# Kernel tuning notes

Hardware: AMD Instinct MI355X
Metric: run time of the kernel (lower is better)

## Reference

```python
import jax, jax.numpy as jnp
import numpy as np

B, S, E, H, F = 8, 1024, 1024, 16, 4096
D = E // H  # head_dim = 64
EPS = 1e-5


def setup_inputs() -> dict:
    key = jax.random.key(0)
    ks = jax.random.split(key, 12)
    s = 0.02
    return {
        "x": jax.random.normal(ks[0], (B, S, E), dtype=jnp.float32),
        # per-head projections (shared across heads), torch stores [out,in]; we use [in,out]
        "Wq": jax.random.normal(ks[1], (D, D), dtype=jnp.float32) * s,
        "Wk": jax.random.normal(ks[2], (D, D), dtype=jnp.float32) * s,
        "Wv": jax.random.normal(ks[3], (D, D), dtype=jnp.float32) * s,
        "Wo": jax.random.normal(ks[4], (E, E), dtype=jnp.float32) * s,
        "bo": jnp.zeros((E,), dtype=jnp.float32),
        "W1": jax.random.normal(ks[5], (E, F), dtype=jnp.float32) * s,
        "b1": jnp.zeros((F,), dtype=jnp.float32),
        "W2": jax.random.normal(ks[6], (F, E), dtype=jnp.float32) * s,
        "b2": jnp.zeros((E,), dtype=jnp.float32),
        "g1": jnp.ones((E,), dtype=jnp.float32),
        "beta1": jnp.zeros((E,), dtype=jnp.float32),
        "g2": jnp.ones((E,), dtype=jnp.float32),
        "beta2": jnp.zeros((E,), dtype=jnp.float32),
    }


def _layer_norm(x, g, b):
    m = jnp.mean(x, axis=-1, keepdims=True)
    v = jnp.mean(jnp.square(x - m), axis=-1, keepdims=True)
    return (x - m) * jax.lax.rsqrt(v + EPS) * g + b


def reference(x, Wq, Wk, Wv, Wo, bo, W1, b1, W2, b2, g1, beta1, g2, beta2):
    b, s, e = x.shape
    # --- attention sublayer (pre-norm) ---
    nx = _layer_norm(x, g1, beta1)
    h = nx.reshape(b, s, H, D)              # [B,S,H,D]
    q = h @ Wq                               # per-head linear, weight shared over heads
    k = h @ Wk
    v = h @ Wv
    energy = jnp.einsum('bqhd,bkhd->bhqk', q, k)  # full [B,H,S,S] scores
    mask = jnp.tril(jnp.ones((s, s), dtype=bool))
    energy = jnp.where(mask, energy, -jnp.inf)
    att = jax.nn.softmax(energy / jnp.sqrt(jnp.float32(e)), axis=-1)  # NOTE: scale by sqrt(embed_dim)
    o = jnp.einsum('bhqk,bkhd->bqhd', att, v).reshape(b, s, e)
    x = x + (o @ Wo + bo)
    # --- MLP sublayer (pre-norm); dropout is identity in eval ---
    nx = _layer_norm(x, g2, beta2)
    x = x + (jax.nn.relu(nx @ W1 + b1) @ W2 + b2)
    return x
```

## Files before the change

kernel.cpp:

```cpp
#include <hip/hip_runtime.h>

typedef unsigned short u16;
typedef __attribute__((ext_vector_type(4))) float f4;
typedef __attribute__((ext_vector_type(8))) short s8v;
typedef __attribute__((ext_vector_type(4))) unsigned short u16x4;

#define DEVINL __device__ __forceinline__

DEVINL float b2f(u16 u) { union { unsigned i; float f; } x; x.i = ((unsigned)u) << 16; return x.f; }
DEVINL u16 f2b(float f) {
  union { float f; unsigned i; } x; x.f = f;
  unsigned r = 0x7FFFu + ((x.i >> 16) & 1u);
  return (u16)((x.i + r) >> 16);
}

#define GLD_LDS16(g, l)                                                        \
  __builtin_amdgcn_global_load_lds((__attribute__((address_space(1))) void*)(g), \
                                   (__attribute__((address_space(3))) void*)(l), 16, 0, 0)

__global__ __launch_bounds__(256) void k_transpose_all(
    const float* __restrict__ Wo, const float* __restrict__ W1,
    const float* __restrict__ W2, const float* __restrict__ Wq,
    const float* __restrict__ Wk, const float* __restrict__ Wv,
    u16* __restrict__ WoT, u16* __restrict__ W1T, u16* __restrict__ W2T,
    u16* __restrict__ WqT, u16* __restrict__ WkT, u16* __restrict__ WvT) {
  int id = blockIdx.x;
  const float* in;
  u16* out;
  int R, C, bx, by;
  if (id < 1024) {
    in = Wo; out = WoT; R = 1024; C = 1024; bx = id & 31; by = id >> 5;
  } else if (id < 5120) {
    int t = id - 1024;
    in = W1; out = W1T; R = 1024; C = 4096; bx = t & 127; by = t >> 7;
  } else if (id < 9216) {
    int t = id - 5120;
    in = W2; out = W2T; R = 4096; C = 1024; bx = t & 31; by = t >> 5;
  } else {
    int t = id - 9216;
    int z = t >> 2;
    in = z == 0 ? Wq : (z == 1 ? Wk : Wv);
    out = z == 0 ? WqT : (z == 1 ? WkT : WvT);
    R = 64; C = 64; bx = t & 1; by = (t >> 1) & 1;
  }
  __shared__ float tt[32][33];
  int tx = threadIdx.x & 31, ty = threadIdx.x >> 5;
  int c0 = bx * 32, r0 = by * 32;
#pragma unroll
  for (int i = 0; i < 32; i += 8)
    tt[ty + i][tx] = in[(long)(r0 + ty + i) * C + (c0 + tx)];
  __syncthreads();
#pragma unroll
  for (int i = 0; i < 32; i += 8)
    out[(long)(c0 + ty + i) * R + (r0 + tx)] = f2b(tt[tx][ty + i]);
}

__global__ __launch_bounds__(256) void k_vtrans(const u16* __restrict__ v, u16* __restrict__ vt) {
  __shared__ u16 t[64][72];
  int bh = blockIdx.x, b = bh >> 4, h = bh & 15;
  int s0 = blockIdx.y * 64;
  int tid = threadIdx.x;
#pragma unroll
  for (int p = 0; p < 2; ++p) {
    int idx = p * 256 + tid;
    int sl = idx >> 3, c8 = (idx & 7) * 8;
    *(s8v*)(&t[sl][c8]) = *(const s8v*)(v + (((long)(b * 1024 + s0 + sl) * 16 + h) * 64) + c8);
  }
  __syncthreads();
#pragma unroll
  for (int p = 0; p < 2; ++p) {
    int idx = p * 256 + tid;
    int d = idx >> 3, c8 = (idx & 7) * 8;
    s8v o;
#pragma unroll
    for (int e = 0; e < 8; ++e) o[e] = (short)t[c8 + e][d];
    *(s8v*)(vt + ((long)bh * 64 + d) * 1024 + s0 + c8) = o;
  }
}

__global__ __launch_bounds__(256) void k_layernorm(const float* __restrict__ x,
                                                   const float* __restrict__ g,
                                                   const float* __restrict__ be,
                                                   u16* __restrict__ out) {
  long row = blockIdx.x;
  int tid = threadIdx.x;
  f4 v = ((const f4*)(x + row * 1024))[tid];
  float s = v[0] + v[1] + v[2] + v[3];
  float s2 = v[0] * v[0] + v[1] * v[1] + v[2] * v[2] + v[3] * v[3];
#pragma unroll
  for (int off = 32; off > 0; off >>= 1) {
    s += __shfl_down(s, off, 64);
    s2 += __shfl_down(s2, off, 64);
  }
  __shared__ float red[8];
  int wv = tid >> 6, ln = tid & 63;
  if (ln == 0) { red[wv] = s; red[4 + wv] = s2; }
  __syncthreads();
  s = red[0] + red[1] + red[2] + red[3];
  s2 = red[4] + red[5] + red[6] + red[7];
  float mean = s * (1.0f / 1024.0f);
  float var = s2 * (1.0f / 1024.0f) - mean * mean;
  float rs = rsqrtf(var + 1e-5f);
  f4 gg = ((const f4*)g)[tid];
  f4 bb = ((const f4*)be)[tid];
  u16x4 o;
#pragma unroll
  for (int i = 0; i < 4; ++i) o[i] = f2b((v[i] - mean) * rs * gg[i] + bb[i]);
  ((u16x4*)(out + row * 1024))[tid] = o;
}

__global__ __launch_bounds__(256) void k_ln_qkv(
    const float* __restrict__ x, const float* __restrict__ g, const float* __restrict__ be,
    const u16* __restrict__ WqT, const u16* __restrict__ WkT, const u16* __restrict__ WvT,
    u16* __restrict__ q, u16* __restrict__ k, u16* __restrict__ v) {
  constexpr int LDP = 72;
  __shared__ u16 A[64 * LDP];
  int tid = threadIdx.x, lane = tid & 63, wave = tid >> 6;
  int quad = lane >> 4, l16 = lane & 15;
  long xrow = (long)blockIdx.x * 4 + wave;
  const f4* xp = (const f4*)(x + xrow * 1024);
  const f4* gp = (const f4*)g;
  const f4* bp = (const f4*)be;
  f4 vv[4];
  float s = 0.f, s2 = 0.f;
#pragma unroll
  for (int j = 0; j < 4; ++j) {
    vv[j] = xp[lane * 4 + j];
#pragma unroll
    for (int e = 0; e < 4; ++e) { s += vv[j][e]; s2 += vv[j][e] * vv[j][e]; }
  }
#pragma unroll
  for (int off = 1; off < 64; off <<= 1) {
    s += __shfl_xor(s, off, 64);
    s2 += __shfl_xor(s2, off, 64);
  }
  float mean = s * (1.0f / 1024.0f);
  float var = s2 * (1.0f / 1024.0f) - mean * mean;
  float rs = rsqrtf(var + 1e-5f);
  u16* ap = &A[(wave * 16 + (lane >> 2)) * LDP + (lane & 3) * 16];
#pragma unroll
  for (int j = 0; j < 4; ++j) {
    f4 gg = gp[lane * 4 + j], bb = bp[lane * 4 + j];
    u16x4 o;
#pragma unroll
    for (int e = 0; e < 4; ++e) o[e] = f2b((vv[j][e] - mean) * rs * gg[e] + bb[e]);
    *(u16x4*)(ap + j * 4) = o;
  }
  __syncthreads();
  s8v a0 = *(const s8v*)(&A[(wave * 16 + l16) * LDP + quad * 8]);
  s8v a1 = *(const s8v*)(&A[(wave * 16 + l16) * LDP + 32 + quad * 8]);
  long rbase = (long)blockIdx.x * 64 + wave * 16;
  const u16* Ws[3] = {WqT, WkT, WvT};
  u16* Os[3] = {q, k, v};
#pragma unroll
  for (int t = 0; t < 3; ++t) {
    f4 acc4[4];
#pragma unroll
    for (int j = 0; j < 4; ++j) {
      s8v b0 = *(const s8v*)(Ws[t] + (j * 16 + l16) * 64 + quad * 8);
      s8v b1 = *(const s8v*)(Ws[t] + (j * 16 + l16) * 64 + 32 + quad * 8);
      f4 acc = {0.f, 0.f, 0.f, 0.f};
      acc = __builtin_amdgcn_mfma_f32_16x16x32_bf16(a0, b0, acc, 0, 0, 0);
      acc = __builtin_amdgcn_mfma_f32_16x16x32_bf16(a1, b1, acc, 0, 0, 0);
      acc4[j] = acc;
    }
    __syncthreads();
#pragma unroll
    for (int j = 0; j < 4; ++j)
#pragma unroll
      for (int r = 0; r < 4; ++r)
        A[(wave * 16 + quad * 4 + r) * LDP + j * 16 + l16] = f2b(acc4[j][r]);
    __syncthreads();
#pragma unroll
    for (int it = 0; it < 2; ++it) {
      int idx = it * 64 + lane;
      int row = idx >> 3, c8 = (idx & 7) * 8;
      s8v v8 = *(const s8v*)(&A[(wave * 16 + row) * LDP + c8]);
      *(s8v*)(Os[t] + (rbase + row) * 64 + c8) = v8;
    }
  }
}

__global__ __launch_bounds__(512) void k_attn_mfma(const u16* __restrict__ q,
                                                   const u16* __restrict__ kk,
                                                   const u16* __restrict__ vt,
                                                   u16* __restrict__ o) {
  constexpr int LDK = 72;
  __shared__ u16 Ks[2][64 * LDK];
  __shared__ u16 Vt[2][64 * LDK];
  __shared__ u16 Ps[8][16 * LDK];
  int tid = threadIdx.x, lane = tid & 63, wave = tid >> 6;
  int quad = lane >> 4, l16 = lane & 15;
  int b = blockIdx.x >> 4, h = blockIdx.x & 15;
  int qi = (int)gridDim.y - 1 - (int)blockIdx.y;
  int q0 = qi * 128 + wave * 16;
  int myNt = 2 * qi + (wave >> 2);
  int lastKt = 2 * qi + 1;

  const u16* qp = q + (((long)(b * 1024 + q0 + l16)) * 16 + h) * 64;
  s8v aq0 = *(const s8v*)(qp + quad * 8);
  s8v aq1 = *(const s8v*)(qp + 32 + quad * 8);

  int srow = tid >> 3, sc8 = (tid & 7) * 8;
  const u16* kb_ = kk + (long)b * 1048576 + h * 64;
  const u16* vb_ = vt + (long)blockIdx.x * 65536;

  f4 O[4];
  float m_[4], l_[4];
#pragma unroll
  for (int jd = 0; jd < 4; ++jd) O[jd] = f4{0.f, 0.f, 0.f, 0.f};
#pragma unroll
  for (int r = 0; r < 4; ++r) { m_[r] = -__builtin_inff(); l_[r] = 0.f; }

  s8v rk0 = *(const s8v*)(kb_ + (long)srow * 1024 + sc8);
  s8v rv0 = *(const s8v*)(vb_ + (long)srow * 1024 + sc8);
  *(s8v*)(&Ks[0][srow * LDK + sc8]) = rk0;
  *(s8v*)(&Vt[0][srow * LDK + sc8]) = rv0;

  for (int kt = 0; kt <= lastKt; ++kt) {
    int cur = kt & 1;
    if (kt < lastKt) {
      long ko = (long)(kt + 1) * 64;
      rk0 = *(const s8v*)(kb_ + (ko + srow) * 1024 + sc8);
      rv0 = *(const s8v*)(vb_ + (long)srow * 1024 + (kt + 1) * 64 + sc8);
    }
    __syncthreads();

    if (kt <= myNt) {
      const u16* Kc = Ks[cur];
      const u16* Vc = Vt[cur];
      f4 sf[4];
      __builtin_amdgcn_s_setprio(1);
#pragma unroll
      for (int jn = 0; jn < 4; ++jn) {
        s8v b0 = *(const s8v*)(Kc + (jn * 16 + l16) * LDK + quad * 8);
        s8v b1 = *(const s8v*)(Kc + (jn * 16 + l16) * LDK + 32 + quad * 8);
        f4 acc = f4{0.f, 0.f, 0.f, 0.f};
        acc = __builtin_amdgcn_mfma_f32_16x16x32_bf16(aq0, b0, acc, 0, 0, 0);
        acc = __builtin_amdgcn_mfma_f32_16x16x32_bf16(aq1, b1, acc, 0, 0, 0);
        sf[jn] = acc;
      }
      __builtin_amdgcn_s_setprio(0);
      bool diag = (kt == myNt);
      int rloc = (wave & 3) * 16 + quad * 4;
      float rm[4];
#pragma unroll
      for (int r = 0; r < 4; ++r) rm[r] = -__builtin_inff();
#pragma unroll
      for (int jn = 0; jn < 4; ++jn)
#pragma unroll
        for (int r = 0; r < 4; ++r) {
          float v = sf[jn][r] * 0.03125f;
          if (diag && (jn * 16 + l16 > rloc + r)) v = -__builtin_inff();
          sf[jn][r] = v;
          rm[r] = fmaxf(rm[r], v);
        }
#pragma unroll
      for (int off = 1; off < 16; off <<= 1)
#pragma unroll
        for (int r = 0; r < 4; ++r) rm[r] = fmaxf(rm[r], __shfl_xor(rm[r], off, 64));
      bool ok = (rm[0] <= m_[0] + 8.f) && (rm[1] <= m_[1] + 8.f) &&
                (rm[2] <= m_[2] + 8.f) && (rm[3] <= m_[3] + 8.f);
      if (!__all(ok)) {
#pragma unroll
        for (int r = 0; r < 4; ++r) {
          float mn = fmaxf(m_[r], rm[r]);
          float alpha = __expf(m_[r] - mn);
          m_[r] = mn;
          l_[r] *= alpha;
#pragma unroll
          for (int jd = 0; jd < 4; ++jd) O[jd][r] *= alpha;
        }
      }
      float rs[4];
#pragma unroll
      for (int r = 0; r < 4; ++r) rs[r] = 0.f;
#pragma unroll
      for (int jn = 0; jn < 4; ++jn)
#pragma unroll
        for (int r = 0; r < 4; ++r) {
          float p = __expf(sf[jn][r] - m_[r]);
          rs[r] += p;
          Ps[wave][(quad * 4 + r) * LDK + jn * 16 + l16] = f2b(p);
        }
#pragma unroll
      for (int off = 1; off < 16; off <<= 1)
#pragma unroll
        for (int r = 0; r < 4; ++r) rs[r] += __shfl_xor(rs[r], off, 64);
#pragma unroll
      for (int r = 0; r < 4; ++r) l_[r] += rs[r];
      asm volatile("s_waitcnt lgkmcnt(0)" ::: "memory");
      s8v p0 = *(const s8v*)(&Ps[wave][l16 * LDK + quad * 8]);
      s8v p1 = *(const s8v*)(&Ps[wave][l16 * LDK + 32 + quad * 8]);
      __builtin_amdgcn_s_setprio(1);
#pragma unroll
      for (int jd = 0; jd < 4; ++jd) {
        s8v b0 = *(const s8v*)(Vc + (jd * 16 + l16) * LDK + quad * 8);
        s8v b1 = *(const s8v*)(Vc + (jd * 16 + l16) * LDK + 32 + quad * 8);
        O[jd] = __builtin_amdgcn_mfma_f32_16x16x32_bf16(p0, b0, O[jd], 0, 0, 0);
        O[jd] = __builtin_amdgcn_mfma_f32_16x16x32_bf16(p1, b1, O[jd], 0, 0, 0);
      }
      __builtin_amdgcn_s_setprio(0);
    }

    if (kt < lastKt) {
      int nb = (cur ^ 1);
      *(s8v*)(&Ks[nb][srow * LDK + sc8]) = rk0;
      *(s8v*)(&Vt[nb][srow * LDK + sc8]) = rv0;
    }
  }
  __syncthreads();
#pragma unroll
  for (int r = 0; r < 4; ++r) {
    float inv = 1.0f / l_[r];
#pragma unroll
    for (int jd = 0; jd < 4; ++jd)
      Ps[wave][(quad * 4 + r) * LDK + jd * 16 + l16] = f2b(O[jd][r] * inv);
  }
  __syncthreads();
#pragma unroll
  for (int it = 0; it < 2; ++it) {
    int idx = it * 64 + lane;
    int row = idx >> 3, c8 = (idx & 7) * 8;
    s8v v8 = *(const s8v*)(&Ps[wave][row * LDK + c8]);
    *(s8v*)(o + (((long)(b * 1024 + q0 + row)) * 16 + h) * 64 + c8) = v8;
  }
}

template <int EPI>
__global__ __launch_bounds__(512) void k_gemm256(const u16* __restrict__ A,
                                                 const u16* __restrict__ BT,
                                                 const float* __restrict__ bias,
                                                 const float* __restrict__ resid,
                                                 void* __restrict__ outp, int M, int N, int K,
                                                 int lda) {
  __shared__ __align__(16) u16 S[65536];
  int tid = threadIdx.x, lane = tid & 63, wave = tid >> 6;
  int l16 = lane & 15, quad = lane >> 4;
  int wm = wave >> 2, wn = wave & 3;
  long bm = blockIdx.x, bn = blockIdx.y;
  int z = blockIdx.z;

  int rl = l16 & 7;
  int c0 = 8 * (quad ^ rl);
  int c1 = 8 * ((quad ^ 4) ^ rl);
  int rowA = (wm * 64 + l16) * 64;
  int rowB = (wn * 32 + l16) * 64;

  int Lb = tid * 16;
  int Ls = Lb ^ (((Lb >> 7) & 7) << 4);
  int r_ = Ls >> 7, kin = (Ls & 127) >> 1;
  const u16* pA = A + (bm * 256 + r_) * (long)lda + kin + (long)z * K;
  const u16* pB = BT + (bn * 256 + r_) * (long)lda + kin + (long)z * K;

  f4 acc[4][4][2];
#pragma unroll
  for (int q = 0; q < 4; ++q)
#pragma unroll
    for (int mi = 0; mi < 4; ++mi)
#pragma unroll
      for (int nj = 0; nj < 2; ++nj) acc[q][mi][nj] = f4{0.f, 0.f, 0.f, 0.f};
  s8v aF[4][2], bF[2][2][2];

#define BAR asm volatile("s_barrier" ::: "memory")
#define LGK0 asm volatile("s_waitcnt lgkmcnt(0)" ::: "memory")
#define WVM4 asm volatile("s_waitcnt vmcnt(4)" ::: "memory")
#define WVM0 asm volatile("s_waitcnt vmcnt(0)" ::: "memory")

#define STAGE(mat, half, t, buf)                                               \
  do {                                                                         \
    const u16* g_ = ((mat) ? pB : pA) + (long)(half) * 128 * lda + (t) * 64;   \
    char* l_ = ((char*)S) + ((buf) * 32768 + (mat) * 16384 + (half) * 8192) * 2 + wave * 1024; \
    GLD_LDS16(g_, l_);                                                         \
    GLD_LDS16(g_ + 64 * (long)lda, l_ + 8192);                                 \
  } while (0)

#define LDA(buf, mh)                                                           \
  do {                                                                         \
    const u16* p_ = S + (buf) * 32768 + (mh) * 8192 + rowA;                    \
    _Pragma("unroll") for (int mi = 0; mi < 4; ++mi) {                         \
      aF[mi][0] = *(const s8v*)(p_ + mi * 1024 + c0);                          \
      aF[mi][1] = *(const s8v*)(p_ + mi * 1024 + c1);                          \
    }                                                                          \
  } while (0)

#define LDB(buf, nh, set)                                                      \
  do {                                                                         \
    const u16* p_ = S + (buf) * 32768 + 16384 + (nh) * 8192 + rowB;            \
    _Pragma("unroll") for (int nj = 0; nj < 2; ++nj) {                         \
      bF[set][nj][0] = *(const s8v*)(p_ + nj * 1024 + c0);                     \
      bF[set][nj][1] = *(const s8v*)(p_ + nj * 1024 + c1);                     \
    }                                                                          \
  } while (0)

#define MM(q)                                                                  \
  do {                                                                         \
    _Pragma("unroll") for (int mi = 0; mi < 4; ++mi)                           \
        _Pragma("unroll") for (int nj = 0; nj < 2; ++nj) {                     \
      acc[q][mi][nj] = __builtin_amdgcn_mfma_f32_16x16x32_bf16(                \
          aF[mi][0], bF[(q) & 1][nj][0], acc[q][mi][nj], 0, 0, 0);             \
      acc[q][mi][nj] = __builtin_amdgcn_mfma_f32_16x16x32_bf16(                \
          aF[mi][1], bF[(q) & 1][nj][1], acc[q][mi][nj], 0, 0, 0);             \
    }                                                                          \
  } while (0)

#define PHASES(t, LAST)                                                        \
  LDA(0, 0); LDB(0, 0, 0); STAGE(0, 1, (t) + 1, 1);                            \
  BAR; LGK0; __builtin_amdgcn_s_setprio(1); MM(0); __builtin_amdgcn_s_setprio(0); BAR; \
  LDB(0, 1, 1); STAGE(1, 1, (t) + 1, 1);                                       \
  BAR; LGK0; __builtin_amdgcn_s_setprio(1); MM(1); __builtin_amdgcn_s_setprio(0); BAR; \
  LDA(0, 1); if (!(LAST)) STAGE(0, 0, (t) + 2, 0);                             \
  BAR; LGK0; __builtin_amdgcn_s_setprio(1); MM(2); __builtin_amdgcn_s_setprio(0); BAR; \
  if (!(LAST)) STAGE(1, 0, (t) + 2, 0);                                        \
  __builtin_amdgcn_s_setprio(1); MM(3); __builtin_amdgcn_s_setprio(0);         \
  if (LAST) { WVM0; } else { WVM4; }                                           \
  BAR;                                                                         \
  LDA(1, 0); LDB(1, 0, 0); if (!(LAST)) STAGE(0, 1, (t) + 2, 0);               \
  BAR; LGK0; __builtin_amdgcn_s_setprio(1); MM(0); __builtin_amdgcn_s_setprio(0); BAR; \
  LDB(1, 1, 1); if (!(LAST)) STAGE(1, 1, (t) + 2, 0);                          \
  BAR; LGK0; __builtin_amdgcn_s_setprio(1); MM(1); __builtin_amdgcn_s_setprio(0); BAR; \
  LDA(1, 1); if (!(LAST)) STAGE(0, 0, (t) + 3, 1);                             \
  BAR; LGK0; __builtin_amdgcn_s_setprio(1); MM(2); __builtin_amdgcn_s_setprio(0); BAR; \
  if (!(LAST)) STAGE(1, 0, (t) + 3, 1);                                        \
  __builtin_amdgcn_s_setprio(1); MM(3); __builtin_amdgcn_s_setprio(0);         \
  if (!(LAST)) { WVM4; BAR; }

  STAGE(0, 0, 0, 0);
  STAGE(1, 0, 0, 0);
  STAGE(0, 1, 0, 0);
  STAGE(1, 1, 0, 0);
  STAGE(0, 0, 1, 1);
  STAGE(1, 0, 1, 1);
  WVM4; BAR;

  int NI = K >> 7;
  for (int i = 0; i < NI - 1; ++i) {
    int t = 2 * i;
    PHASES(t, 0);
  }
  {
    int t = 2 * (NI - 1);
    PHASES(t, 1);
  }

#undef PHASES
#undef MM
#undef LDB
#undef LDA
#undef STAGE
#undef WVM0
#undef WVM4
#undef LGK0
#undef BAR

  if (EPI == 1) {
    __syncthreads();
    int trow = tid >> 4, tcol = (tid & 15) * 8;
#pragma unroll
    for (int q = 0; q < 4; ++q) {
      int mh = q >> 1, nh = q & 1;
#pragma unroll
      for (int nj = 0; nj < 2; ++nj) {
        int c_loc = wn * 32 + nj * 16 + l16;
        float bcol = bias[(int)bn * 256 + nh * 128 + c_loc];
#pragma unroll
        for (int mi = 0; mi < 4; ++mi)
#pragma unroll
          for (int rr = 0; rr < 4; ++rr) {
            int r_loc = wm * 64 + mi * 16 + quad * 4 + rr;
            float val = acc[q][mi][nj][rr] + bcol;
            S[r_loc * 132 + c_loc] = f2b(val > 0.f ? val : 0.f);
          }
      }
      __syncthreads();
#pragma unroll
      for (int p = 0; p < 4; ++p) {
        int r_loc = p * 32 + trow;
        s8v v8 = *(const s8v*)(S + r_loc * 132 + tcol);
        long grow = bm * 256 + mh * 128 + r_loc;
        *(s8v*)((u16*)outp + grow * (long)N + (int)bn * 256 + nh * 128 + tcol) = v8;
      }
      __syncthreads();
    }
  } else {
    float* P0 = (EPI == 0) ? ((float*)outp + (long)z * M * N) : nullptr;
#pragma unroll
    for (int q = 0; q < 4; ++q) {
      int mh = q >> 1, nh = q & 1;
#pragma unroll
      for (int mi = 0; mi < 4; ++mi) {
#pragma unroll
        for (int nj = 0; nj < 2; ++nj) {
          long row = bm * 256 + mh * 128 + wm * 64 + mi * 16 + quad * 4;
          int col = (int)bn * 256 + nh * 128 + wn * 32 + nj * 16 + l16;
#pragma unroll
          for (int rr = 0; rr < 4; ++rr) {
            float val = acc[q][mi][nj][rr];
            if (EPI == 0) {
              P0[(row + rr) * (long)N + col] = val;
            } else {
              ((float*)outp)[(row + rr) * (long)N + col] =
                  resid[(row + rr) * (long)N + col] + val + bias[col];
            }
          }
        }
      }
    }
  }
}

__global__ __launch_bounds__(512) void k_gemm256n128(const u16* __restrict__ A,
                                                     const u16* __restrict__ BT,
                                                     const float* __restrict__ bias,
                                                     const float* __restrict__ resid,
                                                     float* __restrict__ outp,
                                                     int M, int N, int K, int lda) {
  __shared__ __align__(16) u16 S[49152];
  int tid = threadIdx.x, lane = tid & 63, wave = tid >> 6;
  int l16 = lane & 15, quad = lane >> 4;
  int wm = wave >> 1, wn = wave & 1;
  long bm = blockIdx.x, bn = blockIdx.y;

  int rl = l16 & 7;
  int c0 = 8 * (quad ^ rl);
  int c1 = 8 * ((quad ^ 4) ^ rl);
  int rowA = (wm >> 1) * 8192 + ((wm & 1) * 64 + l16) * 64;
  int rowB = 16384 + (wn * 64 + l16) * 64;

  int Lb = tid * 16;
  int Ls = Lb ^ (((Lb >> 7) & 7) << 4);
  int r_ = Ls >> 7, kin = (Ls & 127) >> 1;
  const u16* pA = A + (bm * 256 + r_) * (long)lda + kin;
  const u16* pB = BT + (bn * 128 + r_) * (long)lda + kin;

  f4 acc[4][4];
#pragma unroll
  for (int mi = 0; mi < 4; ++mi)
#pragma unroll
    for (int nj = 0; nj < 4; ++nj) acc[mi][nj] = f4{0.f, 0.f, 0.f, 0.f};
  s8v aF[4][2], bF[2][2];

#define BAR asm volatile("s_barrier" ::: "memory")
#define LGK0 asm volatile("s_waitcnt lgkmcnt(0)" ::: "memory")
#define WVM4 asm volatile("s_waitcnt vmcnt(4)" ::: "memory")
#define WVM0 asm volatile("s_waitcnt vmcnt(0)" ::: "memory")

#define STAGEA(t, buf)                                                         \
  do {                                                                         \
    const u16* g_ = pA + (t) * 64;                                             \
    char* l_ = ((char*)S) + (buf) * 49152 + wave * 1024;                       \
    GLD_LDS16(g_, l_);                                                         \
    GLD_LDS16(g_ + 64 * (long)lda, l_ + 8192);                                 \
    GLD_LDS16(g_ + 128 * (long)lda, l_ + 16384);                               \
    GLD_LDS16(g_ + 192 * (long)lda, l_ + 24576);                               \
  } while (0)

#define STAGEB(t, buf)                                                         \
  do {                                                                         \
    const u16* g_ = pB + (t) * 64;                                             \
    char* l_ = ((char*)S) + (buf) * 49152 + 32768 + wave * 1024;               \
    GLD_LDS16(g_, l_);                                                         \
    GLD_LDS16(g_ + 64 * (long)lda, l_ + 8192);                                 \
  } while (0)

#define LDAn(buf)                                                              \
  do {                                                                         \
    const u16* p_ = S + (buf) * 24576 + rowA;                                  \
    _Pragma("unroll") for (int mi = 0; mi < 4; ++mi) {                         \
      aF[mi][0] = *(const s8v*)(p_ + mi * 1024 + c0);                          \
      aF[mi][1] = *(const s8v*)(p_ + mi * 1024 + c1);                          \
    }                                                                          \
  } while (0)

#define LDBn(buf, nh)                                                          \
  do {                                                                         \
    const u16* p_ = S + (buf) * 24576 + rowB + (nh) * 2048;                    \
    _Pragma("unroll") for (int nj2 = 0; nj2 < 2; ++nj2) {                      \
      bF[nj2][0] = *(const s8v*)(p_ + nj2 * 1024 + c0);                        \
      bF[nj2][1] = *(const s8v*)(p_ + nj2 * 1024 + c1);                        \
    }                                                                          \
  } while (0)

#define MMn(nh)                                                                \
  do {                                                                         \
    _Pragma("unroll") for (int mi = 0; mi < 4; ++mi)                           \
        _Pragma("unroll") for (int nj2 = 0; nj2 < 2; ++nj2) {                  \
      acc[mi][(nh) * 2 + nj2] = __builtin_amdgcn_mfma_f32_16x16x32_bf16(       \
          aF[mi][0], bF[nj2][0], acc[mi][(nh) * 2 + nj2], 0, 0, 0);            \
      acc[mi][(nh) * 2 + nj2] = __builtin_amdgcn_mfma_f32_16x16x32_bf16(       \
          aF[mi][1], bF[nj2][1], acc[mi][(nh) * 2 + nj2], 0, 0, 0);            \
    }                                                                          \
  } while (0)

#define PHASES(t, LAST)                                                        \
  LDAn(0); LDBn(0, 0); STAGEB((t) + 1, 1);                                     \
  BAR; LGK0; __builtin_amdgcn_s_setprio(1); MMn(0); __builtin_amdgcn_s_setprio(0); BAR; \
  LDBn(0, 1); if (!(LAST)) STAGEA((t) + 2, 0);                                 \
  BAR; LGK0; __builtin_amdgcn_s_setprio(1); MMn(1); __builtin_amdgcn_s_setprio(0); \
  if (LAST) { WVM0; } else { WVM4; }                                           \
  BAR;                                                                         \
  LDAn(1); LDBn(1, 0); if (!(LAST)) STAGEB((t) + 2, 0);                        \
  BAR; LGK0; __builtin_amdgcn_s_setprio(1); MMn(0); __builtin_amdgcn_s_setprio(0); BAR; \
  LDBn(1, 1); if (!(LAST)) STAGEA((t) + 3, 1);                                 \
  BAR; LGK0; __builtin_amdgcn_s_setprio(1); MMn(1); __builtin_amdgcn_s_setprio(0); \
  if (!(LAST)) { WVM4; }                                                       \
  BAR;

  STAGEA(0, 0);
  STAGEB(0, 0);
  STAGEA(1, 1);
  WVM4; BAR;

  int NI = K >> 7;
  for (int i = 0; i < NI - 1; ++i) {
    int t = 2 * i;
    PHASES(t, 0);
  }
  {
    int t = 2 * (NI - 1);
    PHASES(t, 1);
  }

#undef PHASES
#undef MMn
#undef LDBn
#undef LDAn
#undef STAGEB
#undef STAGEA
#undef WVM0
#undef WVM4
#undef LGK0
#undef BAR

  __syncthreads();
  float* Sf = (float*)S;
  int halfw = wm >> 1;
  int rbase_loc = (wm & 1) * 64;
#pragma unroll
  for (int h2 = 0; h2 < 2; ++h2) {
    if (halfw == h2) {
#pragma unroll
      for (int mi = 0; mi < 4; ++mi)
#pragma unroll
        for (int nj = 0; nj < 4; ++nj)
#pragma unroll
          for (int rr = 0; rr < 4; ++rr) {
            int r_loc = rbase_loc + mi * 16 + quad * 4 + rr;
            int cc = wn * 64 + nj * 16 + l16;
            Sf[r_loc * 129 + cc] = acc[mi][nj][rr];
          }
    }
    __syncthreads();
#pragma unroll
    for (int p = 0; p < 8; ++p) {
      int idx = p * 512 + tid;
      int r_loc = idx >> 5;
      int cf = (idx & 31) * 4;
      f4 a = *(const f4*)(Sf + r_loc * 129 + cf);
      long grow = bm * 256 + h2 * 128 + r_loc;
      long goff = grow * (long)N + (int)bn * 128 + cf;
      f4 rr4 = *(const f4*)(resid + goff);
      f4 bb4 = *(const f4*)(bias + (int)bn * 128 + cf);
      *(f4*)(outp + goff) = a + rr4 + bb4;
    }
    __syncthreads();
  }
}

extern "C" void kernel_launch(void* const* d_in, const int* in_sizes, int n_in, void* d_out,
                              int out_size, void* d_ws, size_t ws_size, hipStream_t stream) {
  const float* x = (const float*)d_in[0];
  const float* Wq = (const float*)d_in[1];
  const float* Wk = (const float*)d_in[2];
  const float* Wv = (const float*)d_in[3];
  const float* Wo = (const float*)d_in[4];
  const float* bo = (const float*)d_in[5];
  const float* W1 = (const float*)d_in[6];
  const float* b1 = (const float*)d_in[7];
  const float* W2 = (const float*)d_in[8];
  const float* b2 = (const float*)d_in[9];
  const float* g1 = (const float*)d_in[10];
  const float* be1 = (const float*)d_in[11];
  const float* g2 = (const float*)d_in[12];
  const float* be2 = (const float*)d_in[13];

  char* ws = (char*)d_ws;
  const size_t MB = 1ull << 20;
  u16* nx = (u16*)(ws + 0);
  u16* qb = (u16*)(ws + 16 * MB);
  u16* kb = (u16*)(ws + 32 * MB);
  u16* vb = (u16*)(ws + 48 * MB);
  float* x1 = (float*)(ws + 64 * MB);
  u16* h1 = (u16*)(ws + 96 * MB);
  u16* vtr = (u16*)(ws + 96 * MB);
  u16* WoT = (u16*)(ws + 160 * MB);
  u16* W1T = (u16*)(ws + 162 * MB);
  u16* W2T = (u16*)(ws + 170 * MB);
  u16* WqT = (u16*)(ws + 178 * MB);
  u16* WkT = WqT + 64 * 64;
  u16* WvT = WkT + 64 * 64;
  u16* ob = nx;
  u16* nx2 = qb;

  k_transpose_all<<<9228, 256, 0, stream>>>(Wo, W1, W2, Wq, Wk, Wv, WoT, W1T, W2T, WqT, WkT, WvT);

  k_ln_qkv<<<2048, 256, 0, stream>>>(x, g1, be1, WqT, WkT, WvT, qb, kb, vb);
  k_vtrans<<<dim3(128, 16), 256, 0, stream>>>(vb, vtr);
  k_attn_mfma<<<dim3(128, 8), 512, 0, stream>>>(qb, kb, vtr, ob);
  k_gemm256n128<<<dim3(32, 8), 512, 0, stream>>>(ob, WoT, bo, x, x1, 8192, 1024, 1024, 1024);

  k_layernorm<<<8192, 256, 0, stream>>>(x1, g2, be2, nx2);
  k_gemm256<1><<<dim3(32, 16, 1), 512, 0, stream>>>(nx2, W1T, b1, nullptr, h1, 8192, 4096, 1024, 1024);
  k_gemm256n128<<<dim3(32, 8), 512, 0, stream>>>(h1, W2T, b2, x1, (float*)d_out, 8192, 1024, 4096, 4096);
}
```

Baseline: 388.1 us.

## Triple-buffer LDS in 256x128 GEMM kernel for deeper prefetch

```diff
diff --git a/kernel.cpp b/kernel.cpp
--- a/kernel.cpp
+++ b/kernel.cpp
@@ -515,7 +515,7 @@
                                                      const float* __restrict__ resid,
                                                      float* __restrict__ outp,
                                                      int M, int N, int K, int lda) {
-  __shared__ __align__(16) u16 S[49152];
+  __shared__ __align__(16) u16 S[73728];
   int tid = threadIdx.x, lane = tid & 63, wave = tid >> 6;
   int l16 = lane & 15, quad = lane >> 4;
   int wm = wave >> 1, wn = wave & 1;
@@ -544,6 +544,8 @@
 #define LGK0 asm volatile("s_waitcnt lgkmcnt(0)" ::: "memory")
 #define WVM4 asm volatile("s_waitcnt vmcnt(4)" ::: "memory")
 #define WVM0 asm volatile("s_waitcnt vmcnt(0)" ::: "memory")
+#define P1 __builtin_amdgcn_s_setprio(1)
+#define P0 __builtin_amdgcn_s_setprio(0)
 
 #define STAGEA(t, buf)                                                         \
   do {                                                                         \
@@ -592,41 +594,47 @@
     }                                                                          \
   } while (0)
 
-#define PHASES(t, LAST)                                                        \
-  LDAn(0); LDBn(0, 0); STAGEB((t) + 1, 1);                                     \
-  BAR; LGK0; __builtin_amdgcn_s_setprio(1); MMn(0); __builtin_amdgcn_s_setprio(0); BAR; \
-  LDBn(0, 1); if (!(LAST)) STAGEA((t) + 2, 0);                                 \
-  BAR; LGK0; __builtin_amdgcn_s_setprio(1); MMn(1); __builtin_amdgcn_s_setprio(0); \
-  if (LAST) { WVM0; } else { WVM4; }                                           \
-  BAR;                                                                         \
-  LDAn(1); LDBn(1, 0); if (!(LAST)) STAGEB((t) + 2, 0);                        \
-  BAR; LGK0; __builtin_amdgcn_s_setprio(1); MMn(0); __builtin_amdgcn_s_setprio(0); BAR; \
-  LDBn(1, 1); if (!(LAST)) STAGEA((t) + 3, 1);                                 \
-  BAR; LGK0; __builtin_amdgcn_s_setprio(1); MMn(1); __builtin_amdgcn_s_setprio(0); \
-  if (!(LAST)) { WVM4; }                                                       \
-  BAR;
-
   STAGEA(0, 0);
   STAGEB(0, 0);
   STAGEA(1, 1);
+  STAGEB(1, 1);
+  STAGEA(2, 2);
   WVM4; BAR;
 
   int NI = K >> 7;
+  int NT = NI * 2;
+  int ib0 = 0, ib1 = 1, ib2 = 2;
   for (int i = 0; i < NI - 1; ++i) {
     int t = 2 * i;
-    PHASES(t, 0);
+    LDAn(ib0); LDBn(ib0, 0); STAGEB(t + 2, ib2);
+    BAR; LGK0; P1; MMn(0); P0; BAR;
+    LDBn(ib0, 1); STAGEA(t + 3, ib0);
+    BAR; LGK0; P1; MMn(1); P0; WVM4; BAR;
+    LDAn(ib1); LDBn(ib1, 0); STAGEB(t + 3, ib0);
+    BAR; LGK0; P1; MMn(0); P0; BAR;
+    LDBn(ib1, 1); if (t + 4 < NT) STAGEA(t + 4, ib1);
+    BAR; LGK0; P1; MMn(1); P0; WVM4; BAR;
+    int n0 = ib2, n1 = ib0, n2 = ib1;
+    ib0 = n0; ib1 = n1; ib2 = n2;
   }
   {
-    int t = 2 * (NI - 1);
-    PHASES(t, 1);
-  }
-
-#undef PHASES
+    LDAn(ib0); LDBn(ib0, 0);
+    BAR; LGK0; P1; MMn(0); P0; BAR;
+    LDBn(ib0, 1);
+    BAR; LGK0; P1; MMn(1); P0; WVM0; BAR;
+    LDAn(ib1); LDBn(ib1, 0);
+    BAR; LGK0; P1; MMn(0); P0; BAR;
+    LDBn(ib1, 1);
+    BAR; LGK0; P1; MMn(1); P0; BAR;
+  }
+
 #undef MMn
 #undef LDBn
 #undef LDAn
 #undef STAGEB
 #undef STAGEA
+#undef P0
+#undef P1
 #undef WVM0
 #undef WVM4
 #undef LGK0
```

Measured after the change: 392.8 us. About the same (+1.2%).
